# Kernel tuning notes

Measured on AMD Instinct MI355X. Metric: run time of the kernel, lower is better.

The kernel has to match this reference:

```python
import jax, jax.numpy as jnp
import numpy as np

B, C, L, D = 8, 256, 2048, 128  # batch, in_channels, seq_len, n_factor


def setup_inputs() -> dict:
    key = jax.random.key(0)
    ks = jax.random.split(key, 8)
    s = 1.0 / np.sqrt(C)
    return {
        "x_inner": jax.random.normal(ks[0], (B, C, L), jnp.float32),
        "x_outer": jax.random.normal(ks[1], (B, C, L), jnp.float32),
        "Wq": jax.random.normal(ks[2], (D, C), jnp.float32) * s,
        "bq": jax.random.normal(ks[3], (D,), jnp.float32) * 0.01,
        "Wk": jax.random.normal(ks[4], (D, C), jnp.float32) * s,
        "bk": jax.random.normal(ks[5], (D,), jnp.float32) * 0.01,
        "Wv": jax.random.normal(ks[6], (D, C), jnp.float32) * s,
        "bv": jax.random.normal(ks[7], (D,), jnp.float32) * 0.01,
    }


def reference(x_inner, x_outer, Wq, bq, Wk, bk, Wv, bv):
    # kernel-size-1 Conv1d == per-position linear over channels; permute -> [B, L, D]
    q = jnp.einsum('bcl,dc->bld', x_inner, Wq) + bq  # [B, Lq, D]
    k = jnp.einsum('bcl,dc->bld', x_outer, Wk) + bk  # [B, Lk, D]
    v = jnp.einsum('bcl,dc->bld', x_outer, Wv) + bv  # [B, Lk, D]
    scores = jnp.einsum('bqd,bkd->bqk', q, k) / jnp.sqrt(jnp.asarray(D, q.dtype))
    attn = jax.nn.softmax(scores, axis=2)            # [B, Lq, Lk]
    return jnp.einsum('bqk,bkd->bqd', attn, v)       # [B, Lq, D]
```

## Files before the change

kernel.cpp:

```cpp
#include <hip/hip_runtime.h>
#include <hip/hip_bf16.h>

#define NB 8
#define NC 256
#define NL 2048
#define ND 128
#define QKV_ELEMS ((size_t)NB * NL * ND)
#define W_ELEMS (ND * NC)
#define XS_STRIDE 264

typedef __attribute__((ext_vector_type(8))) short bf16x8;
typedef __attribute__((ext_vector_type(4))) float f32x4;
typedef __attribute__((ext_vector_type(16))) float f32x16;
typedef __attribute__((ext_vector_type(4))) unsigned int u32x4;

__device__ __forceinline__ unsigned short f2bf(float f) {
    union { float f; unsigned u; } v; v.f = f;
    unsigned r = v.u + 0x7fffu + ((v.u >> 16) & 1u);
    return (unsigned short)(r >> 16);
}

__device__ __forceinline__ unsigned cvt_pk_bf16(float lo, float hi) {
    unsigned r;
    asm("v_cvt_pk_bf16_f32 %0, %1, %2" : "=v"(r) : "v"(lo), "v"(hi));
    return r;
}

__device__ __forceinline__ void pl32swap(unsigned &a, unsigned &b) {
    asm("v_permlane32_swap_b32 %0, %1" : "+v"(a), "+v"(b));
}

__device__ __forceinline__ void load_lds16(const unsigned short* g, unsigned short* l) {
    __builtin_amdgcn_global_load_lds((const __attribute__((address_space(1))) unsigned int*)g,
                                     (__attribute__((address_space(3))) unsigned int*)l, 16, 0, 0);
}

__global__ void cast_w3(const float* __restrict__ wq, const float* __restrict__ wk,
                        const float* __restrict__ wv, unsigned short* __restrict__ dst) {
    int i = blockIdx.x * blockDim.x + threadIdx.x;
    if (i >= 3 * W_ELEMS) return;
    int sel = i / W_ELEMS, off = i - sel * W_ELEMS;
    const float* s = (sel == 0) ? wq : (sel == 1) ? wk : wv;
    dst[i] = f2bf(s[off]);
}

__device__ __forceinline__ int xs_col(int row, int col) {
    return col ^ (((row >> 2) & 7) << 3);
}

__device__ __forceinline__ void qk_project(const unsigned short* xs, const unsigned short* Wb,
                                           const float* bias, unsigned short* out,
                                           int b, int l0, int wave, int ln, int quad) {
    int m0w = wave * 16;
    f32x4 acc[8] = {};
    int rowq = m0w + ln;
    #pragma unroll
    for (int s = 0; s < 8; s++) {
        bf16x8 af = *reinterpret_cast<const bf16x8*>(xs + rowq * XS_STRIDE + xs_col(rowq, s * 32 + quad * 8));
        #pragma unroll
        for (int t = 0; t < 8; t++) {
            bf16x8 bfr = *reinterpret_cast<const bf16x8*>(Wb + (size_t)(t * 16 + ln) * NC + s * 32 + quad * 8);
            acc[t] = __builtin_amdgcn_mfma_f32_16x16x32_bf16(af, bfr, acc[t], 0, 0, 0);
        }
    }
    #pragma unroll
    for (int t = 0; t < 8; t++) {
        int col = t * 16 + ln;
        float bi = bias[col];
        #pragma unroll
        for (int r = 0; r < 4; r++)
            out[(size_t)(b * NL + l0 + m0w + quad * 4 + r) * ND + col] = f2bf(acc[t][r] + bi);
    }
}

__global__ __launch_bounds__(256, 4) void proj_direct(const float* __restrict__ xi,
                                                      const float* __restrict__ xo,
                                                      const unsigned short* __restrict__ Wall,
                                                      const float* __restrict__ bq,
                                                      const float* __restrict__ bk,
                                                      const float* __restrict__ bv,
                                                      unsigned short* __restrict__ Qb,
                                                      unsigned short* __restrict__ Kb,
                                                      unsigned short* __restrict__ Vtb) {
    __shared__ unsigned short xs[64 * XS_STRIDE];
    int b = blockIdx.x >> 5, lt = blockIdx.x & 31, l0 = lt * 64;
    int y = blockIdx.y;
    int wave = threadIdx.x >> 6, lane = threadIdx.x & 63;
    int ln = lane & 15, quad = lane >> 4;

    const float* xsrc = (y == 0 ? xi : xo) + (size_t)b * NC * NL + l0;
    int l4 = ln * 4;
    #pragma unroll
    for (int G = 0; G < 4; G++) {
        int c0 = G * 64 + wave * 16 + quad * 4;
        float4 r[4];
        #pragma unroll
        for (int cc = 0; cc < 4; cc++)
            r[cc] = *reinterpret_cast<const float4*>(xsrc + (size_t)(c0 + cc) * NL + l4);
        #pragma unroll
        for (int k = 0; k < 4; k++) {
            int row = l4 + k;
            const float* f0 = reinterpret_cast<const float*>(&r[0]);
            const float* f1 = reinterpret_cast<const float*>(&r[1]);
            const float* f2 = reinterpret_cast<const float*>(&r[2]);
            const float* f3 = reinterpret_cast<const float*>(&r[3]);
            uint2 w2 = { cvt_pk_bf16(f0[k], f1[k]), cvt_pk_bf16(f2[k], f3[k]) };
            *reinterpret_cast<uint2*>(&xs[row * XS_STRIDE + xs_col(row, c0)]) = w2;
        }
    }
    __syncthreads();

    if (y == 0) {
        qk_project(xs, Wall, bq, Qb, b, l0, wave, ln, quad);
    } else {
        qk_project(xs, Wall + W_ELEMS, bk, Kb, b, l0, wave, ln, quad);
        const unsigned short* Wb = Wall + 2 * (size_t)W_ELEMS;
        f32x4 acc[2][4] = {};
        #pragma unroll
        for (int s = 0; s < 8; s++) {
            bf16x8 wf0 = *reinterpret_cast<const bf16x8*>(Wb + (size_t)(wave * 32 + ln) * NC + s * 32 + quad * 8);
            bf16x8 wf1 = *reinterpret_cast<const bf16x8*>(Wb + (size_t)(wave * 32 + 16 + ln) * NC + s * 32 + quad * 8);
            #pragma unroll
            for (int t = 0; t < 4; t++) {
                int rowv = t * 16 + ln;
                bf16x8 xb = *reinterpret_cast<const bf16x8*>(xs + rowv * XS_STRIDE + xs_col(rowv, s * 32 + quad * 8));
                acc[0][t] = __builtin_amdgcn_mfma_f32_16x16x32_bf16(wf0, xb, acc[0][t], 0, 0, 0);
                acc[1][t] = __builtin_amdgcn_mfma_f32_16x16x32_bf16(wf1, xb, acc[1][t], 0, 0, 0);
            }
        }
        #pragma unroll
        for (int u = 0; u < 2; u++)
            #pragma unroll
            for (int t = 0; t < 4; t++)
                #pragma unroll
                for (int r = 0; r < 4; r++) {
                    int d = wave * 32 + u * 16 + quad * 4 + r;
                    Vtb[(size_t)(b * ND + d) * NL + l0 + t * 16 + ln] = f2bf(acc[u][t][r] + bv[d]);
                }
    }
}

__global__ __launch_bounds__(512, 1) void flash_attn_one(const unsigned short* __restrict__ Q,
                                                         const unsigned short* __restrict__ K,
                                                         const unsigned short* __restrict__ Vt,
                                                         float* __restrict__ out) {
    __shared__ __align__(16) unsigned short smem[65536];
    unsigned short* kbufp = smem;
    unsigned short* vbufp = smem + 2 * 2 * 64 * 128;
    int bx = blockIdx.x;
    bx = ((bx & 7) << 5) | (bx >> 3);
    int b = bx >> 5, qt = bx & 31;
    int q0 = qt * 64;
    int wave = threadIdx.x >> 6, lane = threadIdx.x & 63;
    int l31 = lane & 31, h = lane >> 5;
    int sp = wave >> 2, wave4 = wave & 3;
    int qg = wave4 >> 1, half = wave4 & 1;
    int kv0 = sp * (NL / 2);
    const float scale = 0.08838834764831845f * 1.4426950408889634f;

    bf16x8 qf[8];
    const unsigned short* qrow = Q + (size_t)(b * NL + q0 + qg * 32 + l31) * ND + h * 8;
    #pragma unroll
    for (int s = 0; s < 8; s++) qf[s] = *reinterpret_cast<const bf16x8*>(qrow + s * 16);

    float lsum = 0.f;
    f32x16 o_acc[4] = {};

    const unsigned short* kg = K + (size_t)b * NL * ND;
    const unsigned short* vg = Vt + (size_t)b * ND * NL;

    int krt = wave4 * 16 + (lane >> 4);
    int kjs = (lane & 15);
    int vdt = wave4 * 32 + (lane >> 3);
    int vjs = (lane & 7);

    {
        unsigned short* kb0 = kbufp + (sp * 2 + 0) * (64 * 128);
        unsigned short* vb0 = vbufp + (sp * 2 + 0) * (128 * 64);
        #pragma unroll
        for (int i = 0; i < 4; i++) {
            int rt = krt + i * 4;
            load_lds16(kg + (size_t)(kv0 + rt) * ND + (kjs ^ (rt & 15)) * 8, kb0 + (wave4 * 16 + i * 4) * 128);
        }
        #pragma unroll
        for (int i = 0; i < 4; i++) {
            int dt = vdt + i * 8;
            load_lds16(vg + (size_t)dt * NL + kv0 + (vjs ^ (dt & 7)) * 8, vb0 + (wave4 * 32 + i * 8) * 64);
        }
    }

    const int niter = (NL / 2) >> 6;
    for (int it = 0; it < niter; it++) {
        int cur = it & 1;
        __syncthreads();

        if (it + 1 < niter) {
            int kt = kv0 + (it + 1) * 64;
            int nxt = cur ^ 1;
            unsigned short* kbn = kbufp + (sp * 2 + nxt) * (64 * 128);
            unsigned short* vbn = vbufp + (sp * 2 + nxt) * (128 * 64);
            #pragma unroll
            for (int i = 0; i < 4; i++) {
                int rt = krt + i * 4;
                load_lds16(kg + (size_t)(kt + rt) * ND + (kjs ^ (rt & 15)) * 8, kbn + (wave4 * 16 + i * 4) * 128);
            }
            #pragma unroll
            for (int i = 0; i < 4; i++) {
                int dt = vdt + i * 8;
                load_lds16(vg + (size_t)dt * NL + kt + (vjs ^ (dt & 7)) * 8, vbn + (wave4 * 32 + i * 8) * 64);
            }
        }
        const unsigned short* kb = kbufp + (sp * 2 + cur) * (64 * 128);
        const unsigned short* vb = vbufp + (sp * 2 + cur) * (128 * 64);

        f32x16 sacc0 = {}, sacc1 = {};
        __builtin_amdgcn_s_setprio(1);
        {
            const unsigned short* krow_p = kb + (half * 32 + l31) * 128;
            #pragma unroll
            for (int s = 0; s < 8; s += 2) {
                bf16x8 kf0 = *reinterpret_cast<const bf16x8*>(krow_p + ((((s + 0) * 2 + h) ^ (l31 & 15)) << 3));
                bf16x8 kf1 = *reinterpret_cast<const bf16x8*>(krow_p + ((((s + 1) * 2 + h) ^ (l31 & 15)) << 3));
                sacc0 = __builtin_amdgcn_mfma_f32_32x32x16_bf16(kf0, qf[s], sacc0, 0, 0, 0);
                sacc1 = __builtin_amdgcn_mfma_f32_32x32x16_bf16(kf1, qf[s + 1], sacc1, 0, 0, 0);
            }
        }
        __builtin_amdgcn_s_setprio(0);

        float p[16];
        #pragma unroll
        for (int g = 0; g < 16; g++) p[g] = __builtin_exp2f((sacc0[g] + sacc1[g]) * scale);
        lsum += (((p[0] + p[1]) + (p[2] + p[3])) + ((p[4] + p[5]) + (p[6] + p[7])))
              + (((p[8] + p[9]) + (p[10] + p[11])) + ((p[12] + p[13]) + (p[14] + p[15])));
        unsigned c0 = cvt_pk_bf16(p[0], p[1]),   c1 = cvt_pk_bf16(p[2], p[3]);
        unsigned c2 = cvt_pk_bf16(p[4], p[5]),   c3 = cvt_pk_bf16(p[6], p[7]);
        unsigned c4 = cvt_pk_bf16(p[8], p[9]),   c5 = cvt_pk_bf16(p[10], p[11]);
        unsigned c6 = cvt_pk_bf16(p[12], p[13]), c7 = cvt_pk_bf16(p[14], p[15]);
        pl32swap(c0, c2); pl32swap(c1, c3);
        pl32swap(c4, c6); pl32swap(c5, c7);
        u32x4 wlo = {c0, c1, c2, c3};
        u32x4 whi = {c4, c5, c6, c7};
        bf16x8 pb0 = __builtin_bit_cast(bf16x8, wlo);
        bf16x8 pb1 = __builtin_bit_cast(bf16x8, whi);

        __builtin_amdgcn_s_setprio(1);
        #pragma unroll
        for (int dt = 0; dt < 4; dt++) {
            const unsigned short* vrow = vb + (dt * 32 + l31) * 64;
            int s0 = half * 2;
            bf16x8 vf0 = *reinterpret_cast<const bf16x8*>(vrow + ((((s0 + 0) * 2 + h) ^ (l31 & 7)) << 3));
            bf16x8 vf1 = *reinterpret_cast<const bf16x8*>(vrow + ((((s0 + 1) * 2 + h) ^ (l31 & 7)) << 3));
            o_acc[dt] = __builtin_amdgcn_mfma_f32_32x32x16_bf16(vf0, pb0, o_acc[dt], 0, 0, 0);
            o_acc[dt] = __builtin_amdgcn_mfma_f32_32x32x16_bf16(vf1, pb1, o_acc[dt], 0, 0, 0);
        }
        __builtin_amdgcn_s_setprio(0);
    }
    lsum += __shfl_xor(lsum, 32);

    __syncthreads();
    float* ored = reinterpret_cast<float*>(smem);
    float* lred = reinterpret_cast<float*>(smem) + 2 * 3 * 128 * 32;
    int idx = sp * 2 + half;
    if (idx > 0) {
        float* o = ored + (qg * 3 + (idx - 1)) * (128 * 32);
        #pragma unroll
        for (int dt = 0; dt < 4; dt++)
            #pragma unroll
            for (int g = 0; g < 4; g++)
                #pragma unroll
                for (int r = 0; r < 4; r++)
                    o[(dt * 32 + g * 8 + h * 4 + r) * 32 + l31] = o_acc[dt][g * 4 + r];
        if (lane < 32) lred[(qg * 3 + (idx - 1)) * 32 + l31] = lsum;
    }
    __syncthreads();
    if (idx == 0) {
        float Lt = lsum + lred[(qg * 3 + 0) * 32 + l31]
                        + lred[(qg * 3 + 1) * 32 + l31]
                        + lred[(qg * 3 + 2) * 32 + l31];
        float inv = 1.0f / Lt;
        int qrow_g = b * NL + q0 + qg * 32 + l31;
        const float* o0 = ored + (qg * 3 + 0) * (128 * 32);
        const float* o1 = ored + (qg * 3 + 1) * (128 * 32);
        const float* o2 = ored + (qg * 3 + 2) * (128 * 32);
        #pragma unroll
        for (int dt = 0; dt < 4; dt++) {
            #pragma unroll
            for (int g = 0; g < 4; g++) {
                f32x4 v4;
                #pragma unroll
                for (int r = 0; r < 4; r++) {
                    int di = (dt * 32 + g * 8 + h * 4 + r) * 32 + l31;
                    v4[r] = (o_acc[dt][g * 4 + r] + o0[di] + o1[di] + o2[di]) * inv;
                }
                *reinterpret_cast<f32x4*>(out + (size_t)qrow_g * ND + dt * 32 + g * 8 + h * 4) = v4;
            }
        }
    }
}

extern "C" void kernel_launch(void* const* d_in, const int* in_sizes, int n_in,
                              void* d_out, int out_size, void* d_ws, size_t ws_size,
                              hipStream_t stream) {
    const float* x_inner = (const float*)d_in[0];
    const float* x_outer = (const float*)d_in[1];
    const float* Wq = (const float*)d_in[2];
    const float* bq = (const float*)d_in[3];
    const float* Wk = (const float*)d_in[4];
    const float* bk = (const float*)d_in[5];
    const float* Wv = (const float*)d_in[6];
    const float* bv = (const float*)d_in[7];
    float* out = (float*)d_out;

    char* w = (char*)d_ws;
    unsigned short* Qb = (unsigned short*)w;
    unsigned short* Kb = Qb + QKV_ELEMS;
    unsigned short* Vtb = Kb + QKV_ELEMS;
    unsigned short* Wall = Vtb + QKV_ELEMS;

    cast_w3<<<(3 * W_ELEMS + 255) / 256, 256, 0, stream>>>(Wq, Wk, Wv, Wall);
    dim3 pgrid(NB * (NL / 64), 2);
    proj_direct<<<pgrid, 256, 0, stream>>>(x_inner, x_outer, Wall, bq, bk, bv, Qb, Kb, Vtb);
    flash_attn_one<<<NB * (NL / 64), 512, 0, stream>>>(Qb, Kb, Vtb, out);
}
```

Baseline: 141.6 us.

## Load K fragments directly to registers and fold softmax scale into Q projection

```diff
diff --git a/kernel.cpp b/kernel.cpp
--- a/kernel.cpp
+++ b/kernel.cpp
@@ -8,6 +8,7 @@
 #define QKV_ELEMS ((size_t)NB * NL * ND)
 #define W_ELEMS (ND * NC)
 #define XS_STRIDE 264
+#define QK_SCALE (0.08838834764831845f * 1.4426950408889634f)
 
 typedef __attribute__((ext_vector_type(8))) short bf16x8;
 typedef __attribute__((ext_vector_type(4))) float f32x4;
@@ -41,7 +42,9 @@
     if (i >= 3 * W_ELEMS) return;
     int sel = i / W_ELEMS, off = i - sel * W_ELEMS;
     const float* s = (sel == 0) ? wq : (sel == 1) ? wk : wv;
-    dst[i] = f2bf(s[off]);
+    float v = s[off];
+    if (sel == 0) v *= QK_SCALE;
+    dst[i] = f2bf(v);
 }
 
 __device__ __forceinline__ int xs_col(int row, int col) {
@@ -50,7 +53,7 @@
 
 __device__ __forceinline__ void qk_project(const unsigned short* xs, const unsigned short* Wb,
                                            const float* bias, unsigned short* out,
-                                           int b, int l0, int wave, int ln, int quad) {
+                                           int b, int l0, int wave, int ln, int quad, float bmul) {
     int m0w = wave * 16;
     f32x4 acc[8] = {};
     int rowq = m0w + ln;
@@ -66,7 +69,7 @@
     #pragma unroll
     for (int t = 0; t < 8; t++) {
         int col = t * 16 + ln;
-        float bi = bias[col];
+        float bi = bias[col] * bmul;
         #pragma unroll
         for (int r = 0; r < 4; r++)
             out[(size_t)(b * NL + l0 + m0w + quad * 4 + r) * ND + col] = f2bf(acc[t][r] + bi);
@@ -111,9 +114,9 @@
     __syncthreads();
 
     if (y == 0) {
-        qk_project(xs, Wall, bq, Qb, b, l0, wave, ln, quad);
+        qk_project(xs, Wall, bq, Qb, b, l0, wave, ln, quad, QK_SCALE);
     } else {
-        qk_project(xs, Wall + W_ELEMS, bk, Kb, b, l0, wave, ln, quad);
+        qk_project(xs, Wall + W_ELEMS, bk, Kb, b, l0, wave, ln, quad, 1.0f);
         const unsigned short* Wb = Wall + 2 * (size_t)W_ELEMS;
         f32x4 acc[2][4] = {};
         #pragma unroll
@@ -140,13 +143,53 @@
     }
 }
 
+__device__ __forceinline__ void flash_step(const bf16x8 (&kreg)[8], const unsigned short* vb,
+                                           const bf16x8 (&qf)[8], f32x16 (&o_acc)[4],
+                                           float& lsum, int l31, int h, int half) {
+    f32x16 sacc0 = {}, sacc1 = {};
+    __builtin_amdgcn_s_setprio(1);
+    #pragma unroll
+    for (int s = 0; s < 8; s += 2) {
+        sacc0 = __builtin_amdgcn_mfma_f32_32x32x16_bf16(kreg[s], qf[s], sacc0, 0, 0, 0);
+        sacc1 = __builtin_amdgcn_mfma_f32_32x32x16_bf16(kreg[s + 1], qf[s + 1], sacc1, 0, 0, 0);
+    }
+    __builtin_amdgcn_s_setprio(0);
+
+    float p[16];
+    #pragma unroll
+    for (int g = 0; g < 16; g++) p[g] = __builtin_exp2f(sacc0[g] + sacc1[g]);
+    lsum += (((p[0] + p[1]) + (p[2] + p[3])) + ((p[4] + p[5]) + (p[6] + p[7])))
+          + (((p[8] + p[9]) + (p[10] + p[11])) + ((p[12] + p[13]) + (p[14] + p[15])));
+    unsigned c0 = cvt_pk_bf16(p[0], p[1]),   c1 = cvt_pk_bf16(p[2], p[3]);
+    unsigned c2 = cvt_pk_bf16(p[4], p[5]),   c3 = cvt_pk_bf16(p[6], p[7]);
+    unsigned c4 = cvt_pk_bf16(p[8], p[9]),   c5 = cvt_pk_bf16(p[10], p[11]);
+    unsigned c6 = cvt_pk_bf16(p[12], p[13]), c7 = cvt_pk_bf16(p[14], p[15]);
+    pl32swap(c0, c2); pl32swap(c1, c3);
+    pl32swap(c4, c6); pl32swap(c5, c7);
+    u32x4 wlo = {c0, c1, c2, c3};
+    u32x4 whi = {c4, c5, c6, c7};
+    bf16x8 pb0 = __builtin_bit_cast(bf16x8, wlo);
+    bf16x8 pb1 = __builtin_bit_cast(bf16x8, whi);
+
+    __builtin_amdgcn_s_setprio(1);
+    #pragma unroll
+    for (int dt = 0; dt < 4; dt++) {
+        const unsigned short* vrow = vb + (dt * 32 + l31) * 64;
+        int s0 = half * 2;
+        bf16x8 vf0 = *reinterpret_cast<const bf16x8*>(vrow + ((((s0 + 0) * 2 + h) ^ (l31 & 7)) << 3));
+        bf16x8 vf1 = *reinterpret_cast<const bf16x8*>(vrow + ((((s0 + 1) * 2 + h) ^ (l31 & 7)) << 3));
+        o_acc[dt] = __builtin_amdgcn_mfma_f32_32x32x16_bf16(vf0, pb0, o_acc[dt], 0, 0, 0);
+        o_acc[dt] = __builtin_amdgcn_mfma_f32_32x32x16_bf16(vf1, pb1, o_acc[dt], 0, 0, 0);
+    }
+    __builtin_amdgcn_s_setprio(0);
+}
+
 __global__ __launch_bounds__(512, 1) void flash_attn_one(const unsigned short* __restrict__ Q,
                                                          const unsigned short* __restrict__ K,
                                                          const unsigned short* __restrict__ Vt,
                                                          float* __restrict__ out) {
-    __shared__ __align__(16) unsigned short smem[65536];
-    unsigned short* kbufp = smem;
-    unsigned short* vbufp = smem + 2 * 2 * 64 * 128;
+    __shared__ __align__(16) unsigned short smem[49152 + 512];
+    unsigned short (*vsm)[2][128 * 64] = reinterpret_cast<unsigned short (*)[2][128 * 64]>(smem);
     int bx = blockIdx.x;
     bx = ((bx & 7) << 5) | (bx >> 3);
     int b = bx >> 5, qt = bx & 31;
@@ -156,7 +199,6 @@
     int sp = wave >> 2, wave4 = wave & 3;
     int qg = wave4 >> 1, half = wave4 & 1;
     int kv0 = sp * (NL / 2);
-    const float scale = 0.08838834764831845f * 1.4426950408889634f;
 
     bf16x8 qf[8];
     const unsigned short* qrow = Q + (size_t)(b * NL + q0 + qg * 32 + l31) * ND + h * 8;
@@ -166,94 +208,60 @@
     float lsum = 0.f;
     f32x16 o_acc[4] = {};
 
-    const unsigned short* kg = K + (size_t)b * NL * ND;
+    const unsigned short* krow0 = K + (size_t)(b * NL + kv0 + half * 32 + l31) * ND + h * 8;
     const unsigned short* vg = Vt + (size_t)b * ND * NL;
-
-    int krt = wave4 * 16 + (lane >> 4);
-    int kjs = (lane & 15);
     int vdt = wave4 * 32 + (lane >> 3);
     int vjs = (lane & 7);
 
+    bf16x8 ka[8], kb_[8];
+
     {
-        unsigned short* kb0 = kbufp + (sp * 2 + 0) * (64 * 128);
-        unsigned short* vb0 = vbufp + (sp * 2 + 0) * (128 * 64);
-        #pragma unroll
-        for (int i = 0; i < 4; i++) {
-            int rt = krt + i * 4;
-            load_lds16(kg + (size_t)(kv0 + rt) * ND + (kjs ^ (rt & 15)) * 8, kb0 + (wave4 * 16 + i * 4) * 128);
-        }
+        unsigned short* vb0 = vsm[sp][0];
         #pragma unroll
         for (int i = 0; i < 4; i++) {
             int dt = vdt + i * 8;
             load_lds16(vg + (size_t)dt * NL + kv0 + (vjs ^ (dt & 7)) * 8, vb0 + (wave4 * 32 + i * 8) * 64);
         }
+        #pragma unroll
+        for (int s = 0; s < 8; s++) ka[s] = *reinterpret_cast<const bf16x8*>(krow0 + s * 16);
     }
 
     const int niter = (NL / 2) >> 6;
-    for (int it = 0; it < niter; it++) {
-        int cur = it & 1;
-        __syncthreads();
-
-        if (it + 1 < niter) {
-            int kt = kv0 + (it + 1) * 64;
-            int nxt = cur ^ 1;
-            unsigned short* kbn = kbufp + (sp * 2 + nxt) * (64 * 128);
-            unsigned short* vbn = vbufp + (sp * 2 + nxt) * (128 * 64);
-            #pragma unroll
-            for (int i = 0; i < 4; i++) {
-                int rt = krt + i * 4;
-                load_lds16(kg + (size_t)(kt + rt) * ND + (kjs ^ (rt & 15)) * 8, kbn + (wave4 * 16 + i * 4) * 128);
+    for (int ip = 0; ip < niter / 2; ip++) {
+        {
+            int it = 2 * ip;
+            __syncthreads();
+            if (it + 1 < niter) {
+                int kt = kv0 + (it + 1) * 64;
+                unsigned short* vbn = vsm[sp][1];
+                #pragma unroll
+                for (int i = 0; i < 4; i++) {
+                    int dt = vdt + i * 8;
+                    load_lds16(vg + (size_t)dt * NL + kt + (vjs ^ (dt & 7)) * 8, vbn + (wave4 * 32 + i * 8) * 64);
+                }
+                const unsigned short* kr = krow0 + (size_t)(it + 1) * 64 * ND;
+                #pragma unroll
+                for (int s = 0; s < 8; s++) kb_[s] = *reinterpret_cast<const bf16x8*>(kr + s * 16);
             }
-            #pragma unroll
-            for (int i = 0; i < 4; i++) {
-                int dt = vdt + i * 8;
-                load_lds16(vg + (size_t)dt * NL + kt + (vjs ^ (dt & 7)) * 8, vbn + (wave4 * 32 + i * 8) * 64);
+            flash_step(ka, vsm[sp][0], qf, o_acc, lsum, l31, h, half);
+        }
+        {
+            int it = 2 * ip + 1;
+            __syncthreads();
+            if (it + 1 < niter) {
+                int kt = kv0 + (it + 1) * 64;
+                unsigned short* vbn = vsm[sp][0];
+                #pragma unroll
+                for (int i = 0; i < 4; i++) {
+                    int dt = vdt + i * 8;
+                    load_lds16(vg + (size_t)dt * NL + kt + (vjs ^ (dt & 7)) * 8, vbn + (wave4 * 32 + i * 8) * 64);
+                }
+                const unsigned short* kr = krow0 + (size_t)(it + 1) * 64 * ND;
+                #pragma unroll
+                for (int s = 0; s < 8; s++) ka[s] = *reinterpret_cast<const bf16x8*>(kr + s * 16);
             }
-        }
-        const unsigned short* kb = kbufp + (sp * 2 + cur) * (64 * 128);
-        const unsigned short* vb = vbufp + (sp * 2 + cur) * (128 * 64);
-
-        f32x16 sacc0 = {}, sacc1 = {};
-        __builtin_amdgcn_s_setprio(1);
-        {
-            const unsigned short* krow_p = kb + (half * 32 + l31) * 128;
-            #pragma unroll
-            for (int s = 0; s < 8; s += 2) {
-                bf16x8 kf0 = *reinterpret_cast<const bf16x8*>(krow_p + ((((s + 0) * 2 + h) ^ (l31 & 15)) << 3));
-                bf16x8 kf1 = *reinterpret_cast<const bf16x8*>(krow_p + ((((s + 1) * 2 + h) ^ (l31 & 15)) << 3));
-                sacc0 = __builtin_amdgcn_mfma_f32_32x32x16_bf16(kf0, qf[s], sacc0, 0, 0, 0);
-                sacc1 = __builtin_amdgcn_mfma_f32_32x32x16_bf16(kf1, qf[s + 1], sacc1, 0, 0, 0);
-            }
-        }
-        __builtin_amdgcn_s_setprio(0);
-
-        float p[16];
-        #pragma unroll
-        for (int g = 0; g < 16; g++) p[g] = __builtin_exp2f((sacc0[g] + sacc1[g]) * scale);
-        lsum += (((p[0] + p[1]) + (p[2] + p[3])) + ((p[4] + p[5]) + (p[6] + p[7])))
-              + (((p[8] + p[9]) + (p[10] + p[11])) + ((p[12] + p[13]) + (p[14] + p[15])));
-        unsigned c0 = cvt_pk_bf16(p[0], p[1]),   c1 = cvt_pk_bf16(p[2], p[3]);
-        unsigned c2 = cvt_pk_bf16(p[4], p[5]),   c3 = cvt_pk_bf16(p[6], p[7]);
-        unsigned c4 = cvt_pk_bf16(p[8], p[9]),   c5 = cvt_pk_bf16(p[10], p[11]);
-        unsigned c6 = cvt_pk_bf16(p[12], p[13]), c7 = cvt_pk_bf16(p[14], p[15]);
-        pl32swap(c0, c2); pl32swap(c1, c3);
-        pl32swap(c4, c6); pl32swap(c5, c7);
-        u32x4 wlo = {c0, c1, c2, c3};
-        u32x4 whi = {c4, c5, c6, c7};
-        bf16x8 pb0 = __builtin_bit_cast(bf16x8, wlo);
-        bf16x8 pb1 = __builtin_bit_cast(bf16x8, whi);
-
-        __builtin_amdgcn_s_setprio(1);
-        #pragma unroll
-        for (int dt = 0; dt < 4; dt++) {
-            const unsigned short* vrow = vb + (dt * 32 + l31) * 64;
-            int s0 = half * 2;
-            bf16x8 vf0 = *reinterpret_cast<const bf16x8*>(vrow + ((((s0 + 0) * 2 + h) ^ (l31 & 7)) << 3));
-            bf16x8 vf1 = *reinterpret_cast<const bf16x8*>(vrow + ((((s0 + 1) * 2 + h) ^ (l31 & 7)) << 3));
-            o_acc[dt] = __builtin_amdgcn_mfma_f32_32x32x16_bf16(vf0, pb0, o_acc[dt], 0, 0, 0);
-            o_acc[dt] = __builtin_amdgcn_mfma_f32_32x32x16_bf16(vf1, pb1, o_acc[dt], 0, 0, 0);
-        }
-        __builtin_amdgcn_s_setprio(0);
+            flash_step(kb_, vsm[sp][1], qf, o_acc, lsum, l31, h, half);
+        }
     }
     lsum += __shfl_xor(lsum, 32);
 
```

Result: slower. 155.7 us (+10.0%).
